# Performance work log

Measured on AMD Instinct MI355X. Metric: run time of the kernel, lower is better.

## Reference

```python
import math
import jax, jax.numpy as jnp
import numpy as np

N = 50000      # nodes
E = 600000     # edges (before self-loops)
D_IN = 64
COND = 32
B = 50         # cond batch; N % B == 0
DT = 128       # dim_t
DH = 128       # dim_h
L = 3          # num GAT layers
FD = 16        # learned_sinusoidal_dim


def setup_inputs() -> dict:
    key = jax.random.key(0)
    ks = jax.random.split(key, 32)
    p = lambda k, shp: (jax.random.normal(k, shp, jnp.float32) * 0.05)
    return {
        "x": jax.random.normal(ks[0], (N, D_IN), jnp.float32),
        "adj": jax.random.randint(ks[1], (2, E), 0, N, dtype=jnp.int32),
        "ef": jax.random.normal(ks[2], (E, 8), jnp.float32),
        "timesteps": jax.random.uniform(ks[3], (N,), jnp.float32) * 1000.0,
        "cond": jax.random.normal(ks[4], (B, COND), jnp.float32),
        # random fourier weights (fixed, not trained in original since is_random=True)
        "fourier_w": jax.random.normal(ks[5], (FD // 2,), jnp.float32),
        # time MLP: Linear(FD+1, DT) -> SiLU -> Linear(DT, DT)
        "tW1": p(ks[6], (FD + 1, DT)), "tb1": p(ks[7], (DT,)),
        "tW2": p(ks[8], (DT, DT)),   "tb2": p(ks[9], (DT,)),
        # conditional projections
        "pxW": p(ks[10], (D_IN, DT)), "pxb": p(ks[11], (DT,)),
        "pcW": p(ks[12], (COND, DT)), "pcb": p(ks[13], (DT,)),
        # stacked GATConv params (all layers 128->128, heads=1)
        "linW": p(ks[14], (L, DT, DH)),   # lin, bias=False
        "attS": p(ks[15], (L, DH)),       # att_src
        "attD": p(ks[16], (L, DH)),       # att_dst
        "gbias": p(ks[17], (L, DH)),      # GATConv bias
        "resW": p(ks[18], (L, DT, DH)),   # residual Linear, bias=False
        # decode MLP
        "dW1": p(ks[19], (DH, DH)), "db1": p(ks[20], (DH,)),
        "dW2": p(ks[21], (DH, 2)),  "db2": p(ks[22], (2,)),
    }


def _gat_layer(h, src, dst, n, linW, attS, attD, gbias, resW):
    # PyG GATConv, heads=1, concat=True, residual=True, add_self_loops already in src/dst
    xl = h @ linW                          # [n, DH]
    a_src = xl @ attS                      # [n]
    a_dst = xl @ attD                      # [n]
    e = jax.nn.leaky_relu(a_src[src] + a_dst[dst], 0.2)   # [E2]
    m = jax.ops.segment_max(e, dst, num_segments=n)
    w = jnp.exp(e - m[dst])
    den = jax.ops.segment_sum(w, dst, num_segments=n)
    alpha = w / den[dst]                   # softmax per destination node
    out = jax.ops.segment_sum(alpha[:, None] * xl[src], dst, num_segments=n)
    return out + gbias + h @ resW


def reference(x, adj, ef, timesteps, cond, fourier_w, tW1, tb1, tW2, tb2,
              pxW, pxb, pcW, pcb, linW, attS, attD, gbias, resW,
              dW1, db1, dW2, db2):
    n = x.shape[0]
    # time embedding: random fourier features, dim = FD + 1
    t = timesteps[:, None]
    freqs = t * fourier_w[None, :] * (2.0 * math.pi)
    four = jnp.concatenate([t, jnp.sin(freqs), jnp.cos(freqs)], axis=-1)
    temb = jax.nn.silu(four @ tW1 + tb1) @ tW2 + tb2
    # conditional projection (cond repeated to match nodes)
    c = jnp.repeat(cond, n // cond.shape[0], axis=0)
    h = (x @ pxW + pxb) + (c @ pcW + pcb) + temb
    # add self-loops once (PyG GATConv default add_self_loops=True)
    loop = jnp.arange(n, dtype=adj.dtype)
    src = jnp.concatenate([adj[0], loop])
    dst = jnp.concatenate([adj[1], loop])
    for l in range(linW.shape[0]):
        h = _gat_layer(h, src, dst, n, linW[l], attS[l], attD[l], gbias[l], resW[l])
        h = jax.nn.gelu(h, approximate=False)
    # decode MLP
    h = jax.nn.gelu(h @ dW1 + db1, approximate=False)
    return h @ dW2 + db2
```

## Files before the change

### kernel.cpp

```cpp
#include <hip/hip_runtime.h>
#include <hip/hip_bf16.h>

#define N_NODES 50000
#define N_EDGES 600000
#define TOT_EDGES (N_EDGES + N_NODES)
#define NPB 1000
#define SCAN_BLK 49

#define PREP_T0 1563
#define PREP_T1 (PREP_T0 + 544)
#define PREP_T2 (PREP_T1 + 3125)
#define PREP_T3 (PREP_T2 + 25)
#define PREP_T4 (PREP_T3 + 3)

typedef __bf16 bf16x8 __attribute__((ext_vector_type(8)));
typedef float f32x4 __attribute__((ext_vector_type(4)));
typedef unsigned short u16x8 __attribute__((ext_vector_type(8)));

__device__ __forceinline__ float gelu_exact(float v){
  return 0.5f * v * (1.f + erff(v * 0.70710678118654752f));
}
__device__ __forceinline__ float silu(float v){
  return v / (1.f + expf(-v));
}
__device__ __forceinline__ unsigned short f2bf(float f){
  unsigned u = __builtin_bit_cast(unsigned, f);
  unsigned r = (u + 0x7FFFu + ((u >> 16) & 1u)) >> 16;
  return (unsigned short)r;
}
__device__ __forceinline__ float bf2f(unsigned short u){
  return __builtin_bit_cast(float, ((unsigned)u) << 16);
}

__global__ __launch_bounds__(256) void count_deg(const int* __restrict__ adj, int* __restrict__ counts){
  int t = blockIdx.x*256 + threadIdx.x;
  if (t >= TOT_EDGES/4) return;
  int j4 = t*4;
  if (j4 < N_EDGES){
    const int4 d4 = *(const int4*)&adj[N_EDGES + j4];
    atomicAdd(&counts[d4.x], 1);
    atomicAdd(&counts[d4.y], 1);
    atomicAdd(&counts[d4.z], 1);
    atomicAdd(&counts[d4.w], 1);
  } else {
    int base = j4 - N_EDGES;
    #pragma unroll
    for (int k = 0; k < 4; k++) atomicAdd(&counts[base+k], 1);
  }
}

__global__ __launch_bounds__(256) void scan_part(const int* __restrict__ counts, int* __restrict__ blksum){
  int tid = threadIdx.x;
  int base = blockIdx.x*1024 + tid*4;
  int s = 0;
  #pragma unroll
  for (int k = 0; k < 4; k++){ int idx = base+k; if (idx < N_NODES) s += counts[idx]; }
  #pragma unroll
  for (int off = 1; off < 64; off <<= 1) s += __shfl_xor(s, off, 64);
  __shared__ int ws[4];
  int lane = tid & 63, wid = tid >> 6;
  if (lane == 0) ws[wid] = s;
  __syncthreads();
  if (tid == 0) blksum[blockIdx.x] = ws[0]+ws[1]+ws[2]+ws[3];
}

__global__ __launch_bounds__(256) void scan_final(const int* __restrict__ counts,
                                                  const int* __restrict__ blksum,
                                                  int* __restrict__ offsets,
                                                  int* __restrict__ cursor){
  int tid = threadIdx.x; int lane = tid & 63, wid = tid >> 6;
  __shared__ int ws[4];
  __shared__ int sbase;
  int base = blockIdx.x*1024 + tid*4;
  int v[4]; int s = 0;
  #pragma unroll
  for (int k = 0; k < 4; k++){ int idx = base+k; v[k] = (idx < N_NODES) ? counts[idx] : 0; s += v[k]; }
  int x = s;
  #pragma unroll
  for (int off = 1; off < 64; off <<= 1){
    int y = __shfl_up(x, off, 64);
    if (lane >= off) x += y;
  }
  if (lane == 63) ws[wid] = x;
  if (tid < 64){
    int bv = (tid < SCAN_BLK) ? blksum[tid] : 0;
    int bx = bv;
    #pragma unroll
    for (int off = 1; off < 64; off <<= 1){
      int y = __shfl_up(bx, off, 64);
      if (tid >= off) bx += y;
    }
    int basev = (blockIdx.x == 0) ? 0 : __shfl(bx, blockIdx.x - 1, 64);
    int total = __shfl(bx, SCAN_BLK - 1, 64);
    if (tid == 0){
      sbase = basev;
      if (blockIdx.x == SCAN_BLK-1) offsets[N_NODES] = total;
    }
  }
  __syncthreads();
  int run = sbase;
  for (int q = 0; q < wid; q++) run += ws[q];
  run += x - s;
  #pragma unroll
  for (int k = 0; k < 4; k++){
    int idx = base+k;
    if (idx < N_NODES){ offsets[idx] = run; cursor[idx] = run; }
    run += v[k];
  }
}

__global__ __launch_bounds__(256) void scatter_edges(const int* __restrict__ adj,
                                                     int* __restrict__ cursor,
                                                     int* __restrict__ srt_src){
  int t = blockIdx.x*256 + threadIdx.x;
  if (t >= TOT_EDGES/4) return;
  int j4 = t*4;
  if (j4 < N_EDGES){
    const int4 s4 = *(const int4*)&adj[j4];
    const int4 d4 = *(const int4*)&adj[N_EDGES + j4];
    int p0 = atomicAdd(&cursor[d4.x], 1); srt_src[p0] = s4.x;
    int p1 = atomicAdd(&cursor[d4.y], 1); srt_src[p1] = s4.y;
    int p2 = atomicAdd(&cursor[d4.z], 1); srt_src[p2] = s4.z;
    int p3 = atomicAdd(&cursor[d4.w], 1); srt_src[p3] = s4.w;
  } else {
    int base = j4 - N_EDGES;
    #pragma unroll
    for (int k = 0; k < 4; k++){
      int d = base + k;
      int pos = atomicAdd(&cursor[d], 1);
      srt_src[pos] = d;
    }
  }
}

__global__ __launch_bounds__(256) void prep_all(const float* __restrict__ timesteps,
                                                const float* __restrict__ fw,
                                                const float* __restrict__ tW1,
                                                const float* __restrict__ tb1,
                                                unsigned short* __restrict__ hid,
                                                const float* __restrict__ linW,
                                                const float* __restrict__ resW,
                                                const float* __restrict__ tW2,
                                                const float* __restrict__ pxW,
                                                const float* __restrict__ dW1,
                                                unsigned short* __restrict__ Bt2,
                                                unsigned short* __restrict__ Bt_init,
                                                unsigned short* __restrict__ Bt_d1,
                                                const float* __restrict__ x,
                                                unsigned short* __restrict__ xbf,
                                                const float* __restrict__ cond,
                                                const float* __restrict__ pcW,
                                                const float* __restrict__ pcb,
                                                float* __restrict__ cproj,
                                                const float* __restrict__ attS,
                                                const float* __restrict__ attD,
                                                float* __restrict__ uv){
  __shared__ float sfour[32][17];
  __shared__ float sW[17][128];
  const int bid = blockIdx.x, tid = threadIdx.x;

  if (bid < PREP_T0){
    int row0 = bid * 32;
    if (tid < 32){
      int gr = row0 + tid;
      float t = (gr < N_NODES) ? timesteps[gr] : 0.f;
      sfour[tid][0] = t;
      #pragma unroll
      for (int q = 0; q < 8; q++){
        float f = t * fw[q] * 6.2831853071795864769f;
        float sv, cv;
        sincosf(f, &sv, &cv);
        sfour[tid][1+q] = sv;
        sfour[tid][9+q] = cv;
      }
    }
    for (int i = tid; i < 17*128; i += 256) sW[i>>7][i&127] = tW1[i];
    __syncthreads();
    int j = tid & 127, rg = tid >> 7;
    float b = tb1[j];
    #pragma unroll
    for (int r = 0; r < 16; r++){
      int row = rg*16 + r;
      float acc = b;
      #pragma unroll
      for (int k = 0; k < 17; k++) acc += sfour[row][k]*sW[k][j];
      int gr = row0 + row;
      if (gr < N_NODES) hid[gr*128 + j] = f2bf(silu(acc));
    }
  } else if (bid < PREP_T1){
    int idx = (bid - PREP_T0)*256 + tid;
    if (idx < 98304){
      int j = idx >> 14, e = idx & 16383;
      int l = j >> 1, isres = j & 1;
      int k = e >> 7, c = e & 127;
      const float* src = (isres ? resW : linW) + l*16384;
      Bt2[(size_t)l*32768 + (size_t)(isres*128 + c)*128 + k] = f2bf(src[k*128 + c]);
    } else if (idx < 114688){
      int e = idx - 98304; int k = e >> 7, c = e & 127;
      Bt_init[c*192 + k] = f2bf(tW2[k*128 + c]);
    } else if (idx < 122880){
      int e = idx - 114688; int k = e >> 7, c = e & 127;
      Bt_init[c*192 + 128 + k] = f2bf(pxW[k*128 + c]);
    } else if (idx < 139264){
      int e = idx - 122880; int k = e >> 7, c = e & 127;
      Bt_d1[c*128 + k] = f2bf(dW1[k*128 + c]);
    }
  } else if (bid < PREP_T2){
    int i = (bid - PREP_T1)*256 + tid;
    float4 v = ((const float4*)x)[i];
    ushort4 o;
    o.x = f2bf(v.x); o.y = f2bf(v.y); o.z = f2bf(v.z); o.w = f2bf(v.w);
    *(ushort4*)&xbf[(size_t)i*4] = o;
  } else if (bid < PREP_T3){
    int g = (bid - PREP_T2)*256 + tid;
    int b = g >> 7, j = g & 127;
    float acc = pcb[j];
    for (int k = 0; k < 32; k++) acc += cond[b*32+k]*pcW[k*128+j];
    cproj[b*128+j] = acc;
  } else {
    int g = (bid - PREP_T3)*256 + tid;
    if (g < 768){
      int l = g >> 8, s = (g >> 7) & 1, k = g & 127;
      const float* att = s ? (attD + l*128) : (attS + l*128);
      const float* row = linW + (l*128 + k)*128;
      float acc = 0.f;
      for (int j = 0; j < 128; j++) acc += row[j]*att[j];
      uv[(l*2 + s)*128 + k] = acc;
    }
  }
}

template<int KD, int EPI, bool SWZ>
__global__ __launch_bounds__(256) void mfma_gemm(const unsigned short* __restrict__ A0,
                                                 const unsigned short* __restrict__ A1,
                                                 const unsigned short* __restrict__ Bt,
                                                 const float* __restrict__ bias0,
                                                 const float* __restrict__ bias1,
                                                 const float* __restrict__ cproj,
                                                 unsigned short* __restrict__ O0,
                                                 unsigned short* __restrict__ O1){
  constexpr int CHR  = KD / 8;
  constexpr int ROWB = KD * 2;
  constexpr int KS   = KD / 32;
  __shared__ alignas(16) char sA[64 * ROWB];
  const int tid  = threadIdx.x;
  int bx, nb;
  if constexpr (SWZ){
    int id = blockIdx.x;
    int nper = gridDim.x >> 3;
    int lin = (id & 7) * nper + (id >> 3);
    bx = lin >> 2; nb = lin & 3;
  } else {
    bx = blockIdx.x; nb = blockIdx.y;
  }
  const int m0   = bx * 64;
  const int lane = tid & 63, w = tid >> 6;
  const int lr   = lane & 15, lk = lane >> 4;

  bf16x8 bfr[4][KS];
  #pragma unroll
  for (int nt = 0; nt < 4; nt++){
    int c = nb*64 + nt*16 + lr;
    #pragma unroll
    for (int ks = 0; ks < KS; ks++)
      bfr[nt][ks] = *(const bf16x8*)&Bt[(size_t)c*KD + ks*32 + lk*8];
  }

  for (int i = tid; i < 64*CHR; i += 256){
    int r = i / CHR, ch = i % CHR;
    int grow = m0 + r;
    u16x8 v;
    #pragma unroll
    for (int q = 0; q < 8; q++) v[q] = 0;
    if (grow < N_NODES){
      if constexpr (KD == 128){
        v = *(const u16x8*)&A0[(size_t)grow*128 + ch*8];
      } else {
        if (ch < 16) v = *(const u16x8*)&A0[(size_t)grow*128 + ch*8];
        else         v = *(const u16x8*)&A1[(size_t)grow*64 + (ch-16)*8];
      }
    }
    *(u16x8*)&sA[r*ROWB + ((ch*16) ^ ((r & 7) << 4))] = v;
  }
  __syncthreads();

  f32x4 acc[4];
  #pragma unroll
  for (int nt = 0; nt < 4; nt++)
    #pragma unroll
    for (int q = 0; q < 4; q++) acc[nt][q] = 0.f;

  const int arow = w*16 + lr;
  #pragma unroll
  for (int ks = 0; ks < KS; ks++){
    bf16x8 a = *(const bf16x8*)&sA[arow*ROWB + ((ks*64 + lk*16) ^ ((arow & 7) << 4))];
    #pragma unroll
    for (int nt = 0; nt < 4; nt++)
      acc[nt] = __builtin_amdgcn_mfma_f32_16x16x32_bf16(a, bfr[nt][ks], acc[nt], 0, 0, 0);
  }

  const int rbase = m0 + w*16 + lk*4;
  #pragma unroll
  for (int nt = 0; nt < 4; nt++){
    int c = nb*64 + nt*16 + lr;
    #pragma unroll
    for (int rg = 0; rg < 4; rg++){
      int row = rbase + rg;
      if (row >= N_NODES) continue;
      float v = acc[nt][rg];
      if constexpr (EPI == 0){
        if (c < 128) O0[(size_t)row*128 + c]       = f2bf(v);
        else         O1[(size_t)row*128 + (c-128)] = f2bf(v);
      } else if constexpr (EPI == 1){
        v += bias0[c] + bias1[c] + cproj[(row/NPB)*128 + c];
        O0[(size_t)row*128 + c] = f2bf(v);
      } else {
        v = gelu_exact(v + bias0[c]);
        O0[(size_t)row*128 + c] = f2bf(v);
      }
    }
  }
}

__global__ __launch_bounds__(256) void dotpair(const unsigned short* __restrict__ h,
                                               const float* __restrict__ uv_l,
                                               float* __restrict__ a_src,
                                               float* __restrict__ a_dst){
  int lane = threadIdx.x & 63, wid = threadIdx.x >> 6;
  int i = blockIdx.x*4 + wid;
  if (i >= N_NODES) return;
  ushort2 hv = *(const ushort2*)&h[(size_t)i*128 + lane*2];
  float h0 = bf2f(hv.x), h1 = bf2f(hv.y);
  float u0 = uv_l[lane*2], u1 = uv_l[lane*2+1];
  float v0 = uv_l[128 + lane*2], v1 = uv_l[128 + lane*2+1];
  float ps = h0*u0 + h1*u1;
  float pd = h0*v0 + h1*v1;
  #pragma unroll
  for (int off = 32; off; off >>= 1){
    ps += __shfl_xor(ps, off, 64);
    pd += __shfl_xor(pd, off, 64);
  }
  if (lane == 0){ a_src[i] = ps; a_dst[i] = pd; }
}

template<bool FUSE>
__global__ __launch_bounds__(256) void aggregate(const unsigned short* __restrict__ xl,
                                                 const float* __restrict__ a_src,
                                                 const float* __restrict__ a_dst,
                                                 const unsigned short* __restrict__ hres,
                                                 const float* __restrict__ gbias_l,
                                                 const int* __restrict__ offsets,
                                                 const int* __restrict__ srt_src,
                                                 unsigned short* __restrict__ h_out,
                                                 const float* __restrict__ uv_next,
                                                 float* __restrict__ a_src_o,
                                                 float* __restrict__ a_dst_o){
  const int tid  = threadIdx.x;
  const int lane = tid & 63;
  const int l16  = lane & 15;
  const int i    = blockIdx.x*16 + (tid >> 4);
  const int beg  = offsets[i];
  const int deg  = offsets[i+1] - beg;
  const float adst = a_dst[i];

  int   s0  = 0;
  float ev0 = -INFINITY;
  if (l16 < deg){
    s0 = srt_src[beg + l16];
    float t = a_src[s0] + adst;
    ev0 = (t > 0.f) ? t : 0.2f*t;
  }
  float m = ev0;
  #pragma unroll
  for (int off = 1; off < 16; off <<= 1) m = fmaxf(m, __shfl_xor(m, off, 64));
  float den = (l16 < deg) ? __expf(ev0 - m) : 0.f;
  #pragma unroll
  for (int off = 1; off < 16; off <<= 1) den += __shfl_xor(den, off, 64);
  for (int c0 = 16; c0 < deg; c0 += 16){
    float ev = -INFINITY;
    if (c0 + l16 < deg){
      int s = srt_src[beg + c0 + l16];
      float t = a_src[s] + adst;
      ev = (t > 0.f) ? t : 0.2f*t;
    }
    float cm = ev;
    #pragma unroll
    for (int off = 1; off < 16; off <<= 1) cm = fmaxf(cm, __shfl_xor(cm, off, 64));
    if (cm > m){ den *= __expf(m - cm); m = cm; }
    float wv = (c0 + l16 < deg) ? __expf(ev - m) : 0.f;
    #pragma unroll
    for (int off = 1; off < 16; off <<= 1) wv += __shfl_xor(wv, off, 64);
    den += wv;
  }
  const float inv = 1.f / den;
  float w0 = (l16 < deg) ? __expf(ev0 - m) * inv : 0.f;

  float acc[8];
  #pragma unroll
  for (int k = 0; k < 8; k++) acc[k] = 0.f;
  const int gbb = (lane & 48) << 2;

  int lim0 = deg < 16 ? deg : 16;
  for (int q = 0; q < lim0; q++){
    int addr = gbb + q*4;
    int s    = __builtin_amdgcn_ds_bpermute(addr, s0);
    float wq = __builtin_bit_cast(float, __builtin_amdgcn_ds_bpermute(addr, __builtin_bit_cast(int, w0)));
    const int4 xv = *(const int4*)&xl[((size_t)s << 7) + (l16 << 3)];
    const int xd[4] = {xv.x, xv.y, xv.z, xv.w};
    #pragma unroll
    for (int k = 0; k < 4; k++){
      acc[2*k]   += wq * __builtin_bit_cast(float, xd[k] << 16);
      acc[2*k+1] += wq * __builtin_bit_cast(float, xd[k] & 0xffff0000);
    }
  }
  for (int c0 = 16; c0 < deg; c0 += 16){
    int s1 = 0; float w1 = 0.f;
    if (c0 + l16 < deg){
      s1 = srt_src[beg + c0 + l16];
      float t = a_src[s1] + adst;
      float ev = (t > 0.f) ? t : 0.2f*t;
      w1 = __expf(ev - m) * inv;
    }
    int lim = deg - c0; if (lim > 16) lim = 16;
    for (int q = 0; q < lim; q++){
      int addr = gbb + q*4;
      int s    = __builtin_amdgcn_ds_bpermute(addr, s1);
      float wq = __builtin_bit_cast(float, __builtin_amdgcn_ds_bpermute(addr, __builtin_bit_cast(int, w1)));
      const int4 xv = *(const int4*)&xl[((size_t)s << 7) + (l16 << 3)];
      const int xd[4] = {xv.x, xv.y, xv.z, xv.w};
      #pragma unroll
      for (int k = 0; k < 4; k++){
        acc[2*k]   += wq * __builtin_bit_cast(float, xd[k] << 16);
        acc[2*k+1] += wq * __builtin_bit_cast(float, xd[k] & 0xffff0000);
      }
    }
  }

  const int4 hr = *(const int4*)&hres[((size_t)i << 7) + (l16 << 3)];
  const int hd[4] = {hr.x, hr.y, hr.z, hr.w};
  const float4 gb0 = *(const float4*)&gbias_l[l16*8];
  const float4 gb1 = *(const float4*)&gbias_l[l16*8 + 4];
  const float gbv[8] = {gb0.x, gb0.y, gb0.z, gb0.w, gb1.x, gb1.y, gb1.z, gb1.w};
  float uu[8], vv[8];
  if constexpr (FUSE){
    const float4 a0 = *(const float4*)&uv_next[l16*8];
    const float4 a1 = *(const float4*)&uv_next[l16*8 + 4];
    const float4 b0 = *(const float4*)&uv_next[128 + l16*8];
    const float4 b1 = *(const float4*)&uv_next[128 + l16*8 + 4];
    uu[0]=a0.x; uu[1]=a0.y; uu[2]=a0.z; uu[3]=a0.w; uu[4]=a1.x; uu[5]=a1.y; uu[6]=a1.z; uu[7]=a1.w;
    vv[0]=b0.x; vv[1]=b0.y; vv[2]=b0.z; vv[3]=b0.w; vv[4]=b1.x; vv[5]=b1.y; vv[6]=b1.z; vv[7]=b1.w;
  }
  float ps = 0.f, pd = 0.f;
  int od[4];
  #pragma unroll
  for (int k = 0; k < 4; k++){
    float r0 = acc[2*k]   + gbv[2*k]   + __builtin_bit_cast(float, hd[k] << 16);
    float r1 = acc[2*k+1] + gbv[2*k+1] + __builtin_bit_cast(float, hd[k] & 0xffff0000);
    float g0 = gelu_exact(r0);
    float g1 = gelu_exact(r1);
    if constexpr (FUSE){
      ps += g0*uu[2*k] + g1*uu[2*k+1];
      pd += g0*vv[2*k] + g1*vv[2*k+1];
    }
    unsigned lo = f2bf(g0);
    unsigned hi = f2bf(g1);
    od[k] = (int)(lo | (hi << 16));
  }
  *(int4*)&h_out[((size_t)i << 7) + (l16 << 3)] = make_int4(od[0], od[1], od[2], od[3]);
  if constexpr (FUSE){
    #pragma unroll
    for (int off = 1; off < 16; off <<= 1){
      ps += __shfl_xor(ps, off, 64);
      pd += __shfl_xor(pd, off, 64);
    }
    if (l16 == 0){ a_src_o[i] = ps; a_dst_o[i] = pd; }
  }
}

__global__ __launch_bounds__(256) void head2(const unsigned short* __restrict__ g,
                                             const float* __restrict__ dW2,
                                             const float* __restrict__ db2,
                                             float* __restrict__ out){
  const int tid = threadIdx.x;
  const int l16 = tid & 15;
  const int i   = blockIdx.x*16 + (tid >> 4);
  const int4 gv = *(const int4*)&g[((size_t)i << 7) + (l16 << 3)];
  const int gd[4] = {gv.x, gv.y, gv.z, gv.w};
  float wk[16];
  #pragma unroll
  for (int q = 0; q < 4; q++){
    const float4 wq = *(const float4*)&dW2[l16*16 + q*4];
    wk[q*4+0]=wq.x; wk[q*4+1]=wq.y; wk[q*4+2]=wq.z; wk[q*4+3]=wq.w;
  }
  float p0 = 0.f, p1 = 0.f;
  #pragma unroll
  for (int k = 0; k < 4; k++){
    float lo = __builtin_bit_cast(float, gd[k] << 16);
    float hi = __builtin_bit_cast(float, gd[k] & 0xffff0000);
    p0 += lo*wk[4*k+0] + hi*wk[4*k+2];
    p1 += lo*wk[4*k+1] + hi*wk[4*k+3];
  }
  #pragma unroll
  for (int off = 1; off < 16; off <<= 1){
    p0 += __shfl_xor(p0, off, 64);
    p1 += __shfl_xor(p1, off, 64);
  }
  if (l16 == 0){
    float2 o; o.x = p0 + db2[0]; o.y = p1 + db2[1];
    *(float2*)&out[i*2] = o;
  }
}

extern "C" void kernel_launch(void* const* d_in, const int* in_sizes, int n_in,
                              void* d_out, int out_size, void* d_ws, size_t ws_size,
                              hipStream_t stream) {
  const float* x   = (const float*)d_in[0];
  const int*   adj = (const int*)  d_in[1];
  const float* timesteps = (const float*)d_in[3];
  const float* cond = (const float*)d_in[4];
  const float* fw   = (const float*)d_in[5];
  const float* tW1  = (const float*)d_in[6];
  const float* tb1  = (const float*)d_in[7];
  const float* tW2  = (const float*)d_in[8];
  const float* tb2  = (const float*)d_in[9];
  const float* pxW  = (const float*)d_in[10];
  const float* pxb  = (const float*)d_in[11];
  const float* pcW  = (const float*)d_in[12];
  const float* pcb  = (const float*)d_in[13];
  const float* linW = (const float*)d_in[14];
  const float* attS = (const float*)d_in[15];
  const float* attD = (const float*)d_in[16];
  const float* gbias= (const float*)d_in[17];
  const float* resW = (const float*)d_in[18];
  const float* dW1  = (const float*)d_in[19];
  const float* db1  = (const float*)d_in[20];
  const float* dW2  = (const float*)d_in[21];
  const float* db2  = (const float*)d_in[22];
  float* out = (float*)d_out;

  char* w = (char*)d_ws;
  size_t off = 0;
  auto carve = [&](size_t bytes) -> void* {
    void* p = w + off;
    off = (off + bytes + 255) & ~(size_t)255;
    return p;
  };
  unsigned short* h_bf    = (unsigned short*)carve((size_t)N_NODES*128*2);
  unsigned short* xl_bf   = (unsigned short*)carve((size_t)N_NODES*128*2);
  unsigned short* hres_bf = (unsigned short*)carve((size_t)N_NODES*128*2);
  unsigned short* x_bf    = (unsigned short*)carve((size_t)N_NODES*64*2);
  float* a_src0 = (float*)carve((size_t)N_NODES*4);
  float* a_dst0 = (float*)carve((size_t)N_NODES*4);
  float* a_src1 = (float*)carve((size_t)N_NODES*4);
  float* a_dst1 = (float*)carve((size_t)N_NODES*4);
  float* cproj = (float*)carve(50*128*4);
  float* uv    = (float*)carve(6*128*4);
  int* counts  = (int*)carve((size_t)N_NODES*4);
  int* cursor  = (int*)carve((size_t)N_NODES*4);
  int* offsets = (int*)carve((size_t)(N_NODES+1)*4);
  int* srt_src = (int*)carve((size_t)TOT_EDGES*4);
  int* blksum  = (int*)carve(SCAN_BLK*4);
  unsigned short* Bt2     = (unsigned short*)carve((size_t)3*256*128*2);
  unsigned short* Bt_init = (unsigned short*)carve((size_t)128*192*2);
  unsigned short* Bt_d1   = (unsigned short*)carve((size_t)128*128*2);
  (void)ws_size; (void)in_sizes; (void)n_in; (void)out_size;

  const int quad_blocks = (TOT_EDGES/4 + 255)/256;
  const int gemm_gx     = (N_NODES + 63)/64;
  const int node_blocks = (N_NODES + 3)/4;
  const int grp_blocks  = N_NODES/16;

  hipMemsetAsync(counts, 0, (size_t)N_NODES*4, stream);
  count_deg<<<quad_blocks, 256, 0, stream>>>(adj, counts);
  scan_part<<<SCAN_BLK, 256, 0, stream>>>(counts, blksum);
  scan_final<<<SCAN_BLK, 256, 0, stream>>>(counts, blksum, offsets, cursor);
  scatter_edges<<<quad_blocks, 256, 0, stream>>>(adj, cursor, srt_src);

  prep_all<<<PREP_T4, 256, 0, stream>>>(timesteps, fw, tW1, tb1, xl_bf ,
                                        linW, resW, tW2, pxW, dW1, Bt2, Bt_init, Bt_d1,
                                        x, x_bf, cond, pcW, pcb, cproj, attS, attD, uv);

  mfma_gemm<192,1,false><<<dim3(gemm_gx,2), 256, 0, stream>>>(xl_bf , x_bf, Bt_init, tb2, pxb, cproj, h_bf, nullptr);

  dotpair<<<node_blocks, 256, 0, stream>>>(h_bf, uv, a_src0, a_dst0);

  float* asrc_in = a_src0; float* adst_in = a_dst0;
  float* asrc_out = a_src1; float* adst_out = a_dst1;
  for (int l = 0; l < 3; l++){
    mfma_gemm<128,0,true><<<gemm_gx*4, 256, 0, stream>>>(h_bf, nullptr, Bt2 + (size_t)l*32768, nullptr, nullptr, nullptr, xl_bf, hres_bf);
    if (l < 2){
      aggregate<true><<<grp_blocks, 256, 0, stream>>>(xl_bf, asrc_in, adst_in, hres_bf, gbias + l*128,
                                                      offsets, srt_src, h_bf, uv + (l+1)*256, asrc_out, adst_out);
      float* t0 = asrc_in; asrc_in = asrc_out; asrc_out = t0;
      float* t1 = adst_in; adst_in = adst_out; adst_out = t1;
    } else {
      aggregate<false><<<grp_blocks, 256, 0, stream>>>(xl_bf, asrc_in, adst_in, hres_bf, gbias + l*128,
                                                       offsets, srt_src, h_bf, nullptr, nullptr, nullptr);
    }
  }

  mfma_gemm<128,2,false><<<dim3(gemm_gx,2), 256, 0, stream>>>(h_bf, nullptr, Bt_d1, db1, nullptr, nullptr, xl_bf , nullptr);
  head2<<<grp_blocks, 256, 0, stream>>>(xl_bf , dW2, db2, out);
}
```

Measured before the change: 471.3 us.

## Build CSR with atomic ranks instead of cursor atomics; fuse attention dots into GEMM

Degree counting now records each edge's atomic return value as its rank within its destination segment. Scatter can then place edges with plain stores at offsets[d]+1+rank instead of a second pass of cursor atomics. Self-loops are handled by adding one to each count and writing the loop entry in the scan. The first layer's attention dot products are computed from the A tile already in shared memory inside the layer-0 GEMM, which removes the separate dotpair launch. The cost is an extra 2.4MB rank buffer written and read back, plus extra work in one GEMM column block.

```diff
diff --git a/kernel.cpp b/kernel.cpp
--- a/kernel.cpp
+++ b/kernel.cpp
@@ -32,21 +32,19 @@
   return __builtin_bit_cast(float, ((unsigned)u) << 16);
 }
 
-__global__ __launch_bounds__(256) void count_deg(const int* __restrict__ adj, int* __restrict__ counts){
+__global__ __launch_bounds__(256) void count_deg(const int* __restrict__ adj,
+                                                 int* __restrict__ counts,
+                                                 int* __restrict__ rank){
   int t = blockIdx.x*256 + threadIdx.x;
-  if (t >= TOT_EDGES/4) return;
+  if (t >= N_EDGES/4) return;
   int j4 = t*4;
-  if (j4 < N_EDGES){
-    const int4 d4 = *(const int4*)&adj[N_EDGES + j4];
-    atomicAdd(&counts[d4.x], 1);
-    atomicAdd(&counts[d4.y], 1);
-    atomicAdd(&counts[d4.z], 1);
-    atomicAdd(&counts[d4.w], 1);
-  } else {
-    int base = j4 - N_EDGES;
-    #pragma unroll
-    for (int k = 0; k < 4; k++) atomicAdd(&counts[base+k], 1);
-  }
+  const int4 d4 = *(const int4*)&adj[N_EDGES + j4];
+  int4 r4;
+  r4.x = atomicAdd(&counts[d4.x], 1);
+  r4.y = atomicAdd(&counts[d4.y], 1);
+  r4.z = atomicAdd(&counts[d4.z], 1);
+  r4.w = atomicAdd(&counts[d4.w], 1);
+  *(int4*)&rank[j4] = r4;
 }
 
 __global__ __launch_bounds__(256) void scan_part(const int* __restrict__ counts, int* __restrict__ blksum){
@@ -54,7 +52,7 @@
   int base = blockIdx.x*1024 + tid*4;
   int s = 0;
   #pragma unroll
-  for (int k = 0; k < 4; k++){ int idx = base+k; if (idx < N_NODES) s += counts[idx]; }
+  for (int k = 0; k < 4; k++){ int idx = base+k; if (idx < N_NODES) s += counts[idx] + 1; }
   #pragma unroll
   for (int off = 1; off < 64; off <<= 1) s += __shfl_xor(s, off, 64);
   __shared__ int ws[4];
@@ -67,14 +65,14 @@
 __global__ __launch_bounds__(256) void scan_final(const int* __restrict__ counts,
                                                   const int* __restrict__ blksum,
                                                   int* __restrict__ offsets,
-                                                  int* __restrict__ cursor){
+                                                  int* __restrict__ srt_src){
   int tid = threadIdx.x; int lane = tid & 63, wid = tid >> 6;
   __shared__ int ws[4];
   __shared__ int sbase;
   int base = blockIdx.x*1024 + tid*4;
   int v[4]; int s = 0;
   #pragma unroll
-  for (int k = 0; k < 4; k++){ int idx = base+k; v[k] = (idx < N_NODES) ? counts[idx] : 0; s += v[k]; }
+  for (int k = 0; k < 4; k++){ int idx = base+k; v[k] = (idx < N_NODES) ? (counts[idx] + 1) : 0; s += v[k]; }
   int x = s;
   #pragma unroll
   for (int off = 1; off < 64; off <<= 1){
@@ -104,33 +102,28 @@
   #pragma unroll
   for (int k = 0; k < 4; k++){
     int idx = base+k;
-    if (idx < N_NODES){ offsets[idx] = run; cursor[idx] = run; }
+    if (idx < N_NODES){
+      offsets[idx] = run;
+      srt_src[run] = idx;
+    }
     run += v[k];
   }
 }
 
 __global__ __launch_bounds__(256) void scatter_edges(const int* __restrict__ adj,
-                                                     int* __restrict__ cursor,
+                                                     const int* __restrict__ rank,
+                                                     const int* __restrict__ offsets,
                                                      int* __restrict__ srt_src){
   int t = blockIdx.x*256 + threadIdx.x;
-  if (t >= TOT_EDGES/4) return;
+  if (t >= N_EDGES/4) return;
   int j4 = t*4;
-  if (j4 < N_EDGES){
-    const int4 s4 = *(const int4*)&adj[j4];
-    const int4 d4 = *(const int4*)&adj[N_EDGES + j4];
-    int p0 = atomicAdd(&cursor[d4.x], 1); srt_src[p0] = s4.x;
-    int p1 = atomicAdd(&cursor[d4.y], 1); srt_src[p1] = s4.y;
-    int p2 = atomicAdd(&cursor[d4.z], 1); srt_src[p2] = s4.z;
-    int p3 = atomicAdd(&cursor[d4.w], 1); srt_src[p3] = s4.w;
-  } else {
-    int base = j4 - N_EDGES;
-    #pragma unroll
-    for (int k = 0; k < 4; k++){
-      int d = base + k;
-      int pos = atomicAdd(&cursor[d], 1);
-      srt_src[pos] = d;
-    }
-  }
+  const int4 s4 = *(const int4*)&adj[j4];
+  const int4 d4 = *(const int4*)&adj[N_EDGES + j4];
+  const int4 r4 = *(const int4*)&rank[j4];
+  srt_src[offsets[d4.x] + 1 + r4.x] = s4.x;
+  srt_src[offsets[d4.y] + 1 + r4.y] = s4.y;
+  srt_src[offsets[d4.z] + 1 + r4.z] = s4.z;
+  srt_src[offsets[d4.w] + 1 + r4.w] = s4.w;
 }
 
 __global__ __launch_bounds__(256) void prep_all(const float* __restrict__ timesteps,
@@ -230,7 +223,7 @@
   }
 }
 
-template<int KD, int EPI, bool SWZ>
+template<int KD, int EPI, bool SWZ, bool DOTS>
 __global__ __launch_bounds__(256) void mfma_gemm(const unsigned short* __restrict__ A0,
                                                  const unsigned short* __restrict__ A1,
                                                  const unsigned short* __restrict__ Bt,
@@ -238,7 +231,10 @@
                                                  const float* __restrict__ bias1,
                                                  const float* __restrict__ cproj,
                                                  unsigned short* __restrict__ O0,
-                                                 unsigned short* __restrict__ O1){
+                                                 unsigned short* __restrict__ O1,
+                                                 const float* __restrict__ uv_l,
+                                                 float* __restrict__ a_srcO,
+                                                 float* __restrict__ a_dstO){
   constexpr int CHR  = KD / 8;
   constexpr int ROWB = KD * 2;
   constexpr int KS   = KD / 32;
@@ -297,6 +293,37 @@
     #pragma unroll
     for (int nt = 0; nt < 4; nt++)
       acc[nt] = __builtin_amdgcn_mfma_f32_16x16x32_bf16(a, bfr[nt][ks], acc[nt], 0, 0, 0);
+  }
+
+  if constexpr (DOTS){
+    if (nb == 0){
+      int r = tid >> 2;
+      int row = m0 + r;
+      if (row < N_NODES){
+        float ps = 0.f, pd = 0.f;
+        #pragma unroll
+        for (int cc = 0; cc < 4; cc++){
+          int ch = (tid & 3)*4 + cc;
+          u16x8 av = *(const u16x8*)&sA[r*ROWB + ((ch*16) ^ ((r & 7) << 4))];
+          int c0 = ch*8;
+          const float4 u0 = *(const float4*)&uv_l[c0];
+          const float4 u1 = *(const float4*)&uv_l[c0+4];
+          const float4 v0 = *(const float4*)&uv_l[128+c0];
+          const float4 v1 = *(const float4*)&uv_l[128+c0+4];
+          const float uu[8] = {u0.x,u0.y,u0.z,u0.w,u1.x,u1.y,u1.z,u1.w};
+          const float vv[8] = {v0.x,v0.y,v0.z,v0.w,v1.x,v1.y,v1.z,v1.w};
+          #pragma unroll
+          for (int q = 0; q < 8; q++){
+            float hv = bf2f(av[q]);
+            ps += hv*uu[q];
+            pd += hv*vv[q];
+          }
+        }
+        ps += __shfl_xor(ps, 1, 64); ps += __shfl_xor(ps, 2, 64);
+        pd += __shfl_xor(pd, 1, 64); pd += __shfl_xor(pd, 2, 64);
+        if ((tid & 3) == 0){ a_srcO[row] = ps; a_dstO[row] = pd; }
+      }
+    }
   }
 
   const int rbase = m0 + w*16 + lk*4;
@@ -320,27 +347,6 @@
       }
     }
   }
-}
-
-__global__ __launch_bounds__(256) void dotpair(const unsigned short* __restrict__ h,
-                                               const float* __restrict__ uv_l,
-                                               float* __restrict__ a_src,
-                                               float* __restrict__ a_dst){
-  int lane = threadIdx.x & 63, wid = threadIdx.x >> 6;
-  int i = blockIdx.x*4 + wid;
-  if (i >= N_NODES) return;
-  ushort2 hv = *(const ushort2*)&h[(size_t)i*128 + lane*2];
-  float h0 = bf2f(hv.x), h1 = bf2f(hv.y);
-  float u0 = uv_l[lane*2], u1 = uv_l[lane*2+1];
-  float v0 = uv_l[128 + lane*2], v1 = uv_l[128 + lane*2+1];
-  float ps = h0*u0 + h1*u1;
-  float pd = h0*v0 + h1*v1;
-  #pragma unroll
-  for (int off = 32; off; off >>= 1){
-    ps += __shfl_xor(ps, off, 64);
-    pd += __shfl_xor(pd, off, 64);
-  }
-  if (lane == 0){ a_src[i] = ps; a_dst[i] = pd; }
 }
 
 template<bool FUSE>
@@ -556,7 +562,7 @@
   float* cproj = (float*)carve(50*128*4);
   float* uv    = (float*)carve(6*128*4);
   int* counts  = (int*)carve((size_t)N_NODES*4);
-  int* cursor  = (int*)carve((size_t)N_NODES*4);
+  int* rank    = (int*)carve((size_t)N_EDGES*4);
   int* offsets = (int*)carve((size_t)(N_NODES+1)*4);
   int* srt_src = (int*)carve((size_t)TOT_EDGES*4);
   int* blksum  = (int*)carve(SCAN_BLK*4);
@@ -565,29 +571,30 @@
   unsigned short* Bt_d1   = (unsigned short*)carve((size_t)128*128*2);
   (void)ws_size; (void)in_sizes; (void)n_in; (void)out_size;
 
-  const int quad_blocks = (TOT_EDGES/4 + 255)/256;
-  const int gemm_gx     = (N_NODES + 63)/64;
-  const int node_blocks = (N_NODES + 3)/4;
-  const int grp_blocks  = N_NODES/16;
+  const int edge4_blocks = (N_EDGES/4 + 255)/256;
+  const int gemm_gx      = (N_NODES + 63)/64;
+  const int grp_blocks   = N_NODES/16;
 
   hipMemsetAsync(counts, 0, (size_t)N_NODES*4, stream);
-  count_deg<<<quad_blocks, 256, 0, stream>>>(adj, counts);
+  count_deg<<<edge4_blocks, 256, 0, stream>>>(adj, counts, rank);
   scan_part<<<SCAN_BLK, 256, 0, stream>>>(counts, blksum);
-  scan_final<<<SCAN_BLK, 256, 0, stream>>>(counts, blksum, offsets, cursor);
-  scatter_edges<<<quad_blocks, 256, 0, stream>>>(adj, cursor, srt_src);
+  scan_final<<<SCAN_BLK, 256, 0, stream>>>(counts, blksum, offsets, srt_src);
+  scatter_edges<<<edge4_blocks, 256, 0, stream>>>(adj, rank, offsets, srt_src);
 
   prep_all<<<PREP_T4, 256, 0, stream>>>(timesteps, fw, tW1, tb1, xl_bf ,
                                         linW, resW, tW2, pxW, dW1, Bt2, Bt_init, Bt_d1,
                                         x, x_bf, cond, pcW, pcb, cproj, attS, attD, uv);
 
-  mfma_gemm<192,1,false><<<dim3(gemm_gx,2), 256, 0, stream>>>(xl_bf , x_bf, Bt_init, tb2, pxb, cproj, h_bf, nullptr);
-
-  dotpair<<<node_blocks, 256, 0, stream>>>(h_bf, uv, a_src0, a_dst0);
+  mfma_gemm<192,1,false,false><<<dim3(gemm_gx,2), 256, 0, stream>>>(xl_bf , x_bf, Bt_init, tb2, pxb, cproj, h_bf, nullptr, nullptr, nullptr, nullptr);
 
   float* asrc_in = a_src0; float* adst_in = a_dst0;
   float* asrc_out = a_src1; float* adst_out = a_dst1;
   for (int l = 0; l < 3; l++){
-    mfma_gemm<128,0,true><<<gemm_gx*4, 256, 0, stream>>>(h_bf, nullptr, Bt2 + (size_t)l*32768, nullptr, nullptr, nullptr, xl_bf, hres_bf);
+    if (l == 0){
+      mfma_gemm<128,0,true,true><<<gemm_gx*4, 256, 0, stream>>>(h_bf, nullptr, Bt2, nullptr, nullptr, nullptr, xl_bf, hres_bf, uv, asrc_in, adst_in);
+    } else {
+      mfma_gemm<128,0,true,false><<<gemm_gx*4, 256, 0, stream>>>(h_bf, nullptr, Bt2 + (size_t)l*32768, nullptr, nullptr, nullptr, xl_bf, hres_bf, nullptr, nullptr, nullptr);
+    }
     if (l < 2){
       aggregate<true><<<grp_blocks, 256, 0, stream>>>(xl_bf, asrc_in, adst_in, hres_bf, gbias + l*128,
                                                       offsets, srt_src, h_bf, uv + (l+1)*256, asrc_out, adst_out);
@@ -599,6 +606,6 @@
     }
   }
 
-  mfma_gemm<128,2,false><<<dim3(gemm_gx,2), 256, 0, stream>>>(h_bf, nullptr, Bt_d1, db1, nullptr, nullptr, xl_bf , nullptr);
+  mfma_gemm<128,2,false,false><<<dim3(gemm_gx,2), 256, 0, stream>>>(h_bf, nullptr, Bt_d1, db1, nullptr, nullptr, xl_bf , nullptr, nullptr, nullptr, nullptr);
   head2<<<grp_blocks, 256, 0, stream>>>(xl_bf , dW2, db2, out);
 }
```

Result: no change. 462.9 us (-1.8%).
